# Optimization experiments

Measured on AMD Instinct MI355X. Metric: run time of the kernel, lower is better.

## Reference

```python
import jax, jax.numpy as jnp
import numpy as np

B, S, DIN, DEG = 256, 51, 512, 50
N = B * S           # 13056 nodes
E = N * DEG         # 652800 edges
NEG_SLOPE = 0.01    # torch leaky_relu default
EPS = 1e-12         # torch F.normalize default eps


def setup_inputs() -> dict:
    key = jax.random.key(0)
    ks = iter(jax.random.split(key, 64))

    def p(shape):
        fan_in = shape[0] if len(shape) > 1 else shape[0]
        return jax.random.normal(next(ks), shape, jnp.float32) / np.sqrt(fan_in)

    inp = {
        "x": jax.random.normal(next(ks), (B, S, DIN), jnp.float32),
        "x_pose": jax.random.normal(next(ks), (B, S, 7), jnp.float32),
        # mlp2: in_feats->256->128->64 (ReLU)
        "m2w1": p((DIN, 256)), "m2b1": jnp.zeros((256,), jnp.float32),
        "m2w2": p((256, 128)), "m2b2": jnp.zeros((128,), jnp.float32),
        "m2w3": p((128, 64)),  "m2b3": jnp.zeros((64,), jnp.float32),
        # mlp3: 7->16->32->64 (ReLU)
        "m3w1": p((7, 16)),   "m3b1": jnp.zeros((16,), jnp.float32),
        "m3w2": p((16, 32)),  "m3b2": jnp.zeros((32,), jnp.float32),
        "m3w3": p((32, 64)),  "m3b3": jnp.zeros((64,), jnp.float32),
        # Encoder: 128->256 (ReLU)
        "encw": p((128, 256)), "encb": jnp.zeros((256,), jnp.float32),
        # edge MLP: 256->256->128->64->1 (leaky_relu, sigmoid at end)
        "ew1": p((256, 256)), "eb1": jnp.zeros((256,), jnp.float32),
        "ew2": p((256, 128)), "eb2": jnp.zeros((128,), jnp.float32),
        "ew3": p((128, 64)),  "eb3": jnp.zeros((64,), jnp.float32),
        "ew4": p((64, 1)),    "eb4": jnp.zeros((1,), jnp.float32),
        # SAGEConv(256,128,'mean'): fc_self, fc_neigh, bias
        "wself": p((256, 128)), "wneigh": p((256, 128)),
        "sageb": jnp.zeros((128,), jnp.float32),
        # Decoder: 128->7
        "decw": p((128, 7)), "decb": jnp.zeros((7,), jnp.float32),
        # graph edges (src -> dst)
        "edge_src": jax.random.randint(next(ks), (E,), 0, N, jnp.int32),
        "edge_dst": jax.random.randint(next(ks), (E,), 0, N, jnp.int32),
    }
    return inp


def reference(x, x_pose,
              m2w1, m2b1, m2w2, m2b2, m2w3, m2b3,
              m3w1, m3b1, m3w2, m3b2, m3w3, m3b3,
              encw, encb,
              ew1, eb1, ew2, eb2, ew3, eb3, ew4, eb4,
              wself, wneigh, sageb, decw, decb,
              edge_src, edge_dst):
    relu = jax.nn.relu
    lrelu = lambda h: jax.nn.leaky_relu(h, NEG_SLOPE)

    # node feature encoders
    h = relu(relu(relu(x @ m2w1 + m2b1) @ m2w2 + m2b2) @ m2w3 + m2b3)        # [B,S,64]
    hp = relu(relu(relu(x_pose @ m3w1 + m3b1) @ m3w2 + m3b2) @ m3w3 + m3b3)  # [B,S,64]
    xn = relu(jnp.concatenate([h, hp], axis=2) @ encw + encb)                # [B,S,256]
    xn = xn.reshape(N, 256)                                                  # node feats

    # apply_edges: score = sigmoid(MLP(h_u - h_v))
    d = xn[edge_src] - xn[edge_dst]                                          # [E,256]
    s = lrelu(d @ ew1 + eb1)
    s = lrelu(s @ ew2 + eb2)
    s = lrelu(s @ ew3 + eb3)
    e = jax.nn.sigmoid(s @ ew4 + eb4)                                        # [E,1]

    # SAGEConv mean aggregation with edge weights: mean over in-edges of e*h_u
    msg = e * xn[edge_src]                                                   # [E,256]
    neigh_sum = jax.ops.segment_sum(msg, edge_dst, num_segments=N)           # [N,256]
    deg = jax.ops.segment_sum(jnp.ones((E,), jnp.float32), edge_dst, num_segments=N)
    neigh = neigh_sum / jnp.maximum(deg, 1.0)[:, None]                       # zero-deg -> 0
    A = xn @ wself + neigh @ wneigh + sageb                                  # [N,128]
    A = A.reshape(B, S, 128)

    est_pose = A @ decw + decb                                               # [B,S,7]
    pos_out = est_pose[:, 0, :3]
    ori_out = est_pose[:, 0, 3:]

    A = lrelu(A)
    A = A / jnp.maximum(jnp.linalg.norm(A, axis=1, keepdims=True), EPS)      # F.normalize dim=1
    return (A, e, pos_out, ori_out)
```

## Files before the change

kernel.cpp:

```cpp
#include <hip/hip_runtime.h>
#include <math.h>

#define B_ 256
#define S_ 51
#define NN (B_*S_)
#define DEG_ 50
#define EE (NN*DEG_)
#define NEG_SLOPE 0.01f
#define EPS_ 1e-12f

#define A_SIZE (NN*128)
#define E_OFF  A_SIZE
#define POS_OFF (A_SIZE + EE)
#define ORI_OFF (POS_OFF + B_*3)

typedef __bf16 bf16x8 __attribute__((ext_vector_type(8)));
typedef __bf16 bf16x4 __attribute__((ext_vector_type(4)));
typedef float  f32x4  __attribute__((ext_vector_type(4)));

typedef __attribute__((address_space(1))) const void GVoid;
typedef __attribute__((address_space(3))) void LVoid;

__device__ __forceinline__ float act_apply(float v, int ACT) {
    if (ACT == 1) return fmaxf(v, 0.0f);
    if (ACT == 2) return v > 0.0f ? v : NEG_SLOPE * v;
    return v;
}

template<int ACT, int ACC>
__global__ __launch_bounds__(256) void gemm_kernel(
    const float* __restrict__ A, int lda,
    const float* __restrict__ W, int ldw,
    const float* __restrict__ bias,
    float* __restrict__ C, int ldc,
    int M, int K, int N)
{
    __shared__ float As[32][68];
    __shared__ float Ws[32][68];

    const int tid = threadIdx.x;
    const int tx = tid & 15;
    const int ty = tid >> 4;
    const int m0 = blockIdx.x * 64;
    const int n0 = blockIdx.y * 64;

    float acc[4][4];
#pragma unroll
    for (int i = 0; i < 4; ++i)
#pragma unroll
        for (int j = 0; j < 4; ++j) acc[i][j] = 0.0f;

    const int ktiles = (K + 31) >> 5;
    for (int kt = 0; kt < ktiles; ++kt) {
        const int k0 = kt << 5;
#pragma unroll
        for (int it = 0; it < 8; ++it) {
            int idx = tid + it * 256;
            int kk = idx & 31;
            int r  = idx >> 5;
            float v = 0.0f;
            int gr = m0 + r, gk = k0 + kk;
            if (gr < M && gk < K) v = A[(size_t)gr * lda + gk];
            As[kk][r] = v;
        }
#pragma unroll
        for (int it = 0; it < 8; ++it) {
            int idx = tid + it * 256;
            int c  = idx & 63;
            int kk = idx >> 6;
            float v = 0.0f;
            int gk = k0 + kk, gc = n0 + c;
            if (gk < K && gc < N) v = W[(size_t)gk * ldw + gc];
            Ws[kk][c] = v;
        }
        __syncthreads();
#pragma unroll
        for (int kk = 0; kk < 32; ++kk) {
            float4 av = *(const float4*)&As[kk][ty * 4];
            float4 wv = *(const float4*)&Ws[kk][tx * 4];
            float a[4] = {av.x, av.y, av.z, av.w};
            float w[4] = {wv.x, wv.y, wv.z, wv.w};
#pragma unroll
            for (int i = 0; i < 4; ++i)
#pragma unroll
                for (int j = 0; j < 4; ++j)
                    acc[i][j] = fmaf(a[i], w[j], acc[i][j]);
        }
        __syncthreads();
    }

#pragma unroll
    for (int i = 0; i < 4; ++i) {
        int row = m0 + ty * 4 + i;
        if (row >= M) continue;
#pragma unroll
        for (int j = 0; j < 4; ++j) {
            int col = n0 + tx * 4 + j;
            if (col >= N) continue;
            float v = acc[i][j];
            if (bias) v += bias[col];
            if (ACC) v += C[(size_t)row * ldc + col];
            C[(size_t)row * ldc + col] = act_apply(v, ACT);
        }
    }
}

__global__ __launch_bounds__(256) void pack_w_kernel(
    const float* __restrict__ W, __bf16* __restrict__ Wp, int K, int N)
{
    int t = blockIdx.x * 256 + threadIdx.x;
    if (t >= K * N) return;
    int j    = t & 7;
    int lane = (t >> 3) & 63;
    int rkt  = t >> 9;
    int KT = K >> 5;
    int kt = rkt % KT;
    int cf = rkt / KT;
    int k = kt * 32 + (lane >> 4) * 8 + j;
    int n = cf * 16 + (lane & 15);
    Wp[t] = (__bf16)W[(size_t)k * N + n];
}

__global__ __launch_bounds__(256) void pack_w2_kernel(
    const float* __restrict__ W, __bf16* __restrict__ Wph, __bf16* __restrict__ Wpl,
    int K, int N)
{
    int t = blockIdx.x * 256 + threadIdx.x;
    if (t >= K * N) return;
    int j    = t & 7;
    int lane = (t >> 3) & 63;
    int rkt  = t >> 9;
    int KT = K >> 5;
    int kt = rkt % KT;
    int cf = rkt / KT;
    int k = kt * 32 + (lane >> 4) * 8 + j;
    int n = cf * 16 + (lane & 15);
    float v = W[(size_t)k * N + n];
    __bf16 h = (__bf16)v;
    Wph[t] = h;
    Wpl[t] = (__bf16)(v - (float)h);
}

template<int K, int BN>
__global__ __launch_bounds__(256) void ygemm_kernel(
    const __bf16* __restrict__ A, const __bf16* __restrict__ Wp,
    __bf16* __restrict__ C, int ldc)
{
    constexpr int NCF = BN / 16;
    __shared__ __bf16 As[128 * 32];

    const int tid  = threadIdx.x;
    const int lane = tid & 63;
    const int w    = tid >> 6;
    const int lg   = lane >> 4;
    const int li   = lane & 15;
    const int n_blk = blockIdx.x * BN;
    const int m_blk = blockIdx.y * 128;

    f32x4 acc[2][NCF];
#pragma unroll
    for (int mf = 0; mf < 2; ++mf)
#pragma unroll
        for (int cf = 0; cf < NCF; ++cf)
#pragma unroll
            for (int r = 0; r < 4; ++r) acc[mf][cf][r] = 0.0f;

    const __bf16* WpBase = Wp + ((size_t)(n_blk / 16) * (K / 32)) * 512 + (size_t)lane * 8;

    for (int kt = 0; kt < K / 32; ++kt) {
#pragma unroll
        for (int i = 0; i < 2; ++i) {
            int slot0 = i * 256 + w * 64;
            int s  = slot0 + lane;
            int r  = s >> 2;
            int sl = s & 3;
            int kb = sl ^ ((r >> 1) & 3);
            const __bf16* g = A + (size_t)(m_blk + r) * K + kt * 32 + kb * 8;
            __builtin_amdgcn_global_load_lds((GVoid*)g,
                                             (LVoid*)((char*)As + (size_t)slot0 * 16),
                                             16, 0, 0);
        }
        bf16x8 bf[NCF];
        const __bf16* Wb = WpBase + (size_t)kt * 512;
#pragma unroll
        for (int cf = 0; cf < NCF; ++cf)
            bf[cf] = *(const bf16x8*)(Wb + (size_t)cf * (K / 32) * 512);

        __syncthreads();

        bf16x8 af[2];
#pragma unroll
        for (int mf = 0; mf < 2; ++mf) {
            int row = w * 32 + mf * 16 + li;
            int sl  = lg ^ ((row >> 1) & 3);
            af[mf] = *(const bf16x8*)((const char*)As + (size_t)row * 64 + sl * 16);
        }
#pragma unroll
        for (int mf = 0; mf < 2; ++mf)
#pragma unroll
            for (int cf = 0; cf < NCF; ++cf)
                acc[mf][cf] = __builtin_amdgcn_mfma_f32_16x16x32_bf16(
                    af[mf], bf[cf], acc[mf][cf], 0, 0, 0);
        __syncthreads();
    }

#pragma unroll
    for (int mf = 0; mf < 2; ++mf) {
        int row0 = m_blk + w * 32 + mf * 16 + lg * 4;
#pragma unroll
        for (int cf = 0; cf < NCF; ++cf) {
            int col = n_blk + cf * 16 + li;
#pragma unroll
            for (int r = 0; r < 4; ++r)
                C[(size_t)(row0 + r) * ldc + col] = (__bf16)acc[mf][cf][r];
        }
    }
}

__global__ __launch_bounds__(256) void edge_fused_kernel(
    const __bf16* __restrict__ Yb, const float* __restrict__ eb1,
    const int* __restrict__ src, const int* __restrict__ dst,
    const __bf16* __restrict__ Wp, const float* __restrict__ eb2,
    __bf16* __restrict__ s2, int e0)
{
    constexpr int K = 256, NCF = 8;
    __shared__ __bf16 As[128 * 32];

    const int tid  = threadIdx.x;
    const int lane = tid & 63;
    const int w    = tid >> 6;
    const int lg   = lane >> 4;
    const int li   = lane & 15;
    const int m_blk = blockIdx.x * 128;

    const int sr = tid >> 1;
    const int sh = tid & 1;
    const int e  = e0 + m_blk + sr;
    const __bf16* ys = Yb + (size_t)src[e] * 256;
    const __bf16* yd = Yb + (size_t)dst[e] * 256;
    const int swz = (sr >> 1) & 3;
    char* wp0 = (char*)As + sr * 64 + (((sh * 2)     ^ swz) * 16);
    char* wp1 = (char*)As + sr * 64 + (((sh * 2 + 1) ^ swz) * 16);

    f32x4 acc[2][NCF];
#pragma unroll
    for (int mf = 0; mf < 2; ++mf)
#pragma unroll
        for (int cf = 0; cf < NCF; ++cf)
#pragma unroll
            for (int r = 0; r < 4; ++r) acc[mf][cf][r] = 0.0f;

    const __bf16* WpBase = Wp + (size_t)lane * 8;

    for (int kt = 0; kt < K / 32; ++kt) {
        const int k0 = kt * 32 + sh * 16;
        bf16x8 a0 = *(const bf16x8*)(ys + k0);
        bf16x8 a1 = *(const bf16x8*)(ys + k0 + 8);
        bf16x8 b0 = *(const bf16x8*)(yd + k0);
        bf16x8 b1 = *(const bf16x8*)(yd + k0 + 8);
        bf16x8 o0, o1;
#pragma unroll
        for (int j = 0; j < 8; ++j) {
            float v0 = (float)a0[j] - (float)b0[j] + eb1[k0 + j];
            float v1 = (float)a1[j] - (float)b1[j] + eb1[k0 + 8 + j];
            v0 = v0 > 0.0f ? v0 : NEG_SLOPE * v0;
            v1 = v1 > 0.0f ? v1 : NEG_SLOPE * v1;
            o0[j] = (__bf16)v0;
            o1[j] = (__bf16)v1;
        }
        *(bf16x8*)wp0 = o0;
        *(bf16x8*)wp1 = o1;

        bf16x8 bf[NCF];
        const __bf16* Wb = WpBase + (size_t)kt * 512;
#pragma unroll
        for (int cf = 0; cf < NCF; ++cf)
            bf[cf] = *(const bf16x8*)(Wb + (size_t)cf * (K / 32) * 512);

        __syncthreads();

        bf16x8 af[2];
#pragma unroll
        for (int mf = 0; mf < 2; ++mf) {
            int row = w * 32 + mf * 16 + li;
            int sl  = lg ^ ((row >> 1) & 3);
            af[mf] = *(const bf16x8*)((const char*)As + (size_t)row * 64 + sl * 16);
        }
#pragma unroll
        for (int mf = 0; mf < 2; ++mf)
#pragma unroll
            for (int cf = 0; cf < NCF; ++cf)
                acc[mf][cf] = __builtin_amdgcn_mfma_f32_16x16x32_bf16(
                    af[mf], bf[cf], acc[mf][cf], 0, 0, 0);
        __syncthreads();
    }

    float bv[NCF];
#pragma unroll
    for (int cf = 0; cf < NCF; ++cf) bv[cf] = eb2[cf * 16 + li];
#pragma unroll
    for (int mf = 0; mf < 2; ++mf) {
        int row0 = m_blk + w * 32 + mf * 16 + lg * 4;
#pragma unroll
        for (int cf = 0; cf < NCF; ++cf) {
            int col = cf * 16 + li;
#pragma unroll
            for (int r = 0; r < 4; ++r) {
                float v = acc[mf][cf][r] + bv[cf];
                v = v > 0.0f ? v : NEG_SLOPE * v;
                s2[(size_t)(row0 + r) * 128 + col] = (__bf16)v;
            }
        }
    }
}

__global__ __launch_bounds__(256) void edge_l3e_kernel(
    const __bf16* __restrict__ A, const __bf16* __restrict__ Wp,
    const float* __restrict__ eb3, const float* __restrict__ ew4,
    const float* __restrict__ eb4, float* __restrict__ e_out, int e0)
{
    constexpr int K = 128, NCF = 4;
    __shared__ __bf16 As[128 * 32];

    const int tid  = threadIdx.x;
    const int lane = tid & 63;
    const int w    = tid >> 6;
    const int lg   = lane >> 4;
    const int li   = lane & 15;
    const int m_blk = blockIdx.y * 128;

    f32x4 acc[2][NCF];
#pragma unroll
    for (int mf = 0; mf < 2; ++mf)
#pragma unroll
        for (int cf = 0; cf < NCF; ++cf)
#pragma unroll
            for (int r = 0; r < 4; ++r) acc[mf][cf][r] = 0.0f;

    const __bf16* WpBase = Wp + (size_t)lane * 8;

    for (int kt = 0; kt < K / 32; ++kt) {
#pragma unroll
        for (int i = 0; i < 2; ++i) {
            int slot0 = i * 256 + w * 64;
            int s  = slot0 + lane;
            int r  = s >> 2;
            int sl = s & 3;
            int kb = sl ^ ((r >> 1) & 3);
            const __bf16* g = A + (size_t)(m_blk + r) * K + kt * 32 + kb * 8;
            __builtin_amdgcn_global_load_lds((GVoid*)g,
                                             (LVoid*)((char*)As + (size_t)slot0 * 16),
                                             16, 0, 0);
        }
        bf16x8 bf[NCF];
        const __bf16* Wb = WpBase + (size_t)kt * 512;
#pragma unroll
        for (int cf = 0; cf < NCF; ++cf)
            bf[cf] = *(const bf16x8*)(Wb + (size_t)cf * (K / 32) * 512);

        __syncthreads();

        bf16x8 af[2];
#pragma unroll
        for (int mf = 0; mf < 2; ++mf) {
            int row = w * 32 + mf * 16 + li;
            int sl  = lg ^ ((row >> 1) & 3);
            af[mf] = *(const bf16x8*)((const char*)As + (size_t)row * 64 + sl * 16);
        }
#pragma unroll
        for (int mf = 0; mf < 2; ++mf)
#pragma unroll
            for (int cf = 0; cf < NCF; ++cf)
                acc[mf][cf] = __builtin_amdgcn_mfma_f32_16x16x32_bf16(
                    af[mf], bf[cf], acc[mf][cf], 0, 0, 0);
        __syncthreads();
    }

    float p[2][4];
#pragma unroll
    for (int mf = 0; mf < 2; ++mf)
#pragma unroll
        for (int r = 0; r < 4; ++r) p[mf][r] = 0.0f;
#pragma unroll
    for (int cf = 0; cf < NCF; ++cf) {
        int col = cf * 16 + li;
        float b3 = eb3[col];
        float w4 = ew4[col];
#pragma unroll
        for (int mf = 0; mf < 2; ++mf)
#pragma unroll
            for (int r = 0; r < 4; ++r) {
                float v = acc[mf][cf][r] + b3;
                v = v > 0.0f ? v : NEG_SLOPE * v;
                p[mf][r] = fmaf(v, w4, p[mf][r]);
            }
    }
#pragma unroll
    for (int mf = 0; mf < 2; ++mf)
#pragma unroll
        for (int r = 0; r < 4; ++r) {
#pragma unroll
            for (int m = 1; m < 16; m <<= 1)
                p[mf][r] += __shfl_xor(p[mf][r], m, 16);
        }
    if (li == 0) {
        float b4 = eb4[0];
#pragma unroll
        for (int mf = 0; mf < 2; ++mf)
#pragma unroll
            for (int r = 0; r < 4; ++r) {
                int ei = m_blk + w * 32 + mf * 16 + lg * 4 + r;
                float ev = 1.0f / (1.0f + expf(-(p[mf][r] + b4)));
                e_out[e0 + ei] = ev;
            }
    }
}

template<int K, int BN, int ACT, int OUT, int ACC>
__global__ __launch_bounds__(256) void mmx_kernel(
    const __bf16* __restrict__ Ah, const __bf16* __restrict__ Al,
    const __bf16* __restrict__ Wph, const __bf16* __restrict__ Wpl,
    const float* __restrict__ bias,
    float* __restrict__ Cf, __bf16* __restrict__ Ch, __bf16* __restrict__ Cl, int ldc)
{
    constexpr int NCF = BN / 16;
    __shared__ __bf16 AsH[128 * 32];
    __shared__ __bf16 AsL[128 * 32];

    const int tid  = threadIdx.x;
    const int lane = tid & 63;
    const int w    = tid >> 6;
    const int lg   = lane >> 4;
    const int li   = lane & 15;
    const int n_blk = blockIdx.x * BN;
    const int m_blk = blockIdx.y * 128;

    f32x4 acc[2][NCF];
#pragma unroll
    for (int mf = 0; mf < 2; ++mf)
#pragma unroll
        for (int cf = 0; cf < NCF; ++cf)
#pragma unroll
            for (int r = 0; r < 4; ++r) acc[mf][cf][r] = 0.0f;

    const size_t wbase = ((size_t)(n_blk / 16) * (K / 32)) * 512 + (size_t)lane * 8;

    for (int kt = 0; kt < K / 32; ++kt) {
#pragma unroll
        for (int i = 0; i < 2; ++i) {
            int slot0 = i * 256 + w * 64;
            int s  = slot0 + lane;
            int r  = s >> 2;
            int sl = s & 3;
            int kb = sl ^ ((r >> 1) & 3);
            size_t goff = (size_t)(m_blk + r) * K + kt * 32 + kb * 8;
            __builtin_amdgcn_global_load_lds((GVoid*)(Ah + goff),
                                             (LVoid*)((char*)AsH + (size_t)slot0 * 16),
                                             16, 0, 0);
            __builtin_amdgcn_global_load_lds((GVoid*)(Al + goff),
                                             (LVoid*)((char*)AsL + (size_t)slot0 * 16),
                                             16, 0, 0);
        }
        bf16x8 bfh[NCF], bfl[NCF];
        const size_t wo = wbase + (size_t)kt * 512;
#pragma unroll
        for (int cf = 0; cf < NCF; ++cf) {
            size_t o = wo + (size_t)cf * (K / 32) * 512;
            bfh[cf] = *(const bf16x8*)(Wph + o);
            bfl[cf] = *(const bf16x8*)(Wpl + o);
        }

        __syncthreads();

        bf16x8 afh[2], afl[2];
#pragma unroll
        for (int mf = 0; mf < 2; ++mf) {
            int row = w * 32 + mf * 16 + li;
            int sl  = lg ^ ((row >> 1) & 3);
            afh[mf] = *(const bf16x8*)((const char*)AsH + (size_t)row * 64 + sl * 16);
            afl[mf] = *(const bf16x8*)((const char*)AsL + (size_t)row * 64 + sl * 16);
        }
#pragma unroll
        for (int mf = 0; mf < 2; ++mf)
#pragma unroll
            for (int cf = 0; cf < NCF; ++cf) {
                acc[mf][cf] = __builtin_amdgcn_mfma_f32_16x16x32_bf16(
                    afh[mf], bfh[cf], acc[mf][cf], 0, 0, 0);
                acc[mf][cf] = __builtin_amdgcn_mfma_f32_16x16x32_bf16(
                    afh[mf], bfl[cf], acc[mf][cf], 0, 0, 0);
                acc[mf][cf] = __builtin_amdgcn_mfma_f32_16x16x32_bf16(
                    afl[mf], bfh[cf], acc[mf][cf], 0, 0, 0);
            }
        __syncthreads();
    }

    float bv[NCF];
#pragma unroll
    for (int cf = 0; cf < NCF; ++cf) bv[cf] = bias ? bias[n_blk + cf * 16 + li] : 0.0f;
#pragma unroll
    for (int mf = 0; mf < 2; ++mf) {
        int row0 = m_blk + w * 32 + mf * 16 + lg * 4;
#pragma unroll
        for (int cf = 0; cf < NCF; ++cf) {
            int col = n_blk + cf * 16 + li;
#pragma unroll
            for (int r = 0; r < 4; ++r) {
                float v = acc[mf][cf][r] + bv[cf];
                size_t idx = (size_t)(row0 + r) * ldc + col;
                if (ACC) v += Cf[idx];
                v = act_apply(v, ACT);
                if (OUT & 1) Cf[idx] = v;
                if (OUT & 2) {
                    __bf16 h = (__bf16)v;
                    Ch[idx] = h;
                    Cl[idx] = (__bf16)(v - (float)h);
                }
            }
        }
    }
}

__global__ __launch_bounds__(256) void split_bf16_kernel(
    const float* __restrict__ in, __bf16* __restrict__ hi, __bf16* __restrict__ lo, int n8)
{
    int i = blockIdx.x * 256 + threadIdx.x;
    if (i >= n8) return;
    const float4* p = (const float4*)in + (size_t)i * 2;
    float4 a = p[0], b = p[1];
    float v[8] = {a.x, a.y, a.z, a.w, b.x, b.y, b.z, b.w};
    bf16x8 oh, ol;
#pragma unroll
    for (int j = 0; j < 8; ++j) {
        __bf16 h = (__bf16)v[j];
        oh[j] = h;
        ol[j] = (__bf16)(v[j] - (float)h);
    }
    *(bf16x8*)(hi + (size_t)i * 8) = oh;
    *(bf16x8*)(lo + (size_t)i * 8) = ol;
}

__global__ __launch_bounds__(256) void hist_kernel(
    const int* __restrict__ dst, int* __restrict__ counts)
{
    int e = blockIdx.x * 256 + threadIdx.x;
    if (e < EE) atomicAdd(&counts[dst[e]], 1);
}

__global__ __launch_bounds__(1024) void scan_kernel(
    const int* __restrict__ counts, int* __restrict__ row_start, int* __restrict__ cursor)
{
    __shared__ int buf[1024];
    __shared__ int carry_s;
    int tid = threadIdx.x;
    if (tid == 0) carry_s = 0;
    __syncthreads();
    for (int t0 = 0; t0 < NN; t0 += 1024) {
        int i = t0 + tid;
        int v = (i < NN) ? counts[i] : 0;
        buf[tid] = v;
        __syncthreads();
        int c = carry_s;
        for (int o = 1; o < 1024; o <<= 1) {
            int u = (tid >= o) ? buf[tid - o] : 0;
            __syncthreads();
            buf[tid] += u;
            __syncthreads();
        }
        int excl = buf[tid] - v;
        if (i < NN) { row_start[i] = c + excl; cursor[i] = c + excl; }
        int total = buf[1023];
        __syncthreads();
        if (tid == 0) carry_s = c + total;
        __syncthreads();
    }
}

__global__ __launch_bounds__(256) void scatter_kernel(
    const int* __restrict__ src, const int* __restrict__ dst,
    const float* __restrict__ e_out, int* __restrict__ cursor, int2* __restrict__ bucket)
{
    int e = blockIdx.x * 256 + threadIdx.x;
    if (e >= EE) return;
    int d = dst[e];
    int pos = atomicAdd(&cursor[d], 1);
    bucket[pos] = make_int2(src[e], __float_as_int(e_out[e]));
}

__global__ __launch_bounds__(256) void neigh_gather_kernel(
    const float* __restrict__ xn, const int2* __restrict__ bucket,
    const int* __restrict__ row_start, const int* __restrict__ counts,
    __bf16* __restrict__ nh, __bf16* __restrict__ nl)
{
    __shared__ int2 eb[128];
    int n = blockIdx.x;
    int f = threadIdx.x;
    int s0 = row_start[n];
    int cnt = counts[n];
    float acc = 0.0f;
    for (int t = 0; t < cnt; t += 128) {
        int m = (cnt - t < 128) ? (cnt - t) : 128;
        __syncthreads();
        if (f < m) eb[f] = bucket[s0 + t + f];
        __syncthreads();
        for (int i = 0; i < m; ++i) {
            int2 p = eb[i];
            acc = fmaf(__int_as_float(p.y), xn[(size_t)p.x * 256 + f], acc);
        }
    }
    float dv = (float)(cnt > 0 ? cnt : 1);
    float v = acc / dv;
    __bf16 h = (__bf16)v;
    nh[(size_t)n * 256 + f] = h;
    nl[(size_t)n * 256 + f] = (__bf16)(v - (float)h);
}

__global__ __launch_bounds__(128) void pose_kernel(
    const float* __restrict__ A_pre, const float* __restrict__ decw,
    const float* __restrict__ decb, float* __restrict__ pos, float* __restrict__ ori)
{
    __shared__ float arow[128];
    int b = blockIdx.x;
    arow[threadIdx.x] = A_pre[(size_t)(b * S_) * 128 + threadIdx.x];
    __syncthreads();
    int t = threadIdx.x;
    if (t < 7) {
        float s = decb[t];
        for (int c = 0; c < 128; ++c) s = fmaf(arow[c], decw[c * 7 + t], s);
        if (t < 3) pos[b * 3 + t] = s;
        else       ori[b * 4 + (t - 3)] = s;
    }
}

__global__ __launch_bounds__(128) void norm_kernel(
    const float* __restrict__ A_pre, float* __restrict__ out)
{
    int b = blockIdx.x;
    int c = threadIdx.x;
    size_t base = (size_t)b * S_ * 128 + c;
    float ss = 0.0f;
    for (int s = 0; s < S_; ++s) {
        float v = A_pre[base + (size_t)s * 128];
        v = v > 0.0f ? v : NEG_SLOPE * v;
        ss = fmaf(v, v, ss);
    }
    float nrm = fmaxf(sqrtf(ss), EPS_);
    float inv = 1.0f / nrm;
    for (int s = 0; s < S_; ++s) {
        float v = A_pre[base + (size_t)s * 128];
        v = v > 0.0f ? v : NEG_SLOPE * v;
        out[base + (size_t)s * 128] = v * inv;
    }
}

extern "C" void kernel_launch(void* const* d_in, const int* in_sizes, int n_in,
                              void* d_out, int out_size, void* d_ws, size_t ws_size,
                              hipStream_t stream) {
    const float* x      = (const float*)d_in[0];
    const float* x_pose = (const float*)d_in[1];
    const float* m2w1 = (const float*)d_in[2];
    const float* m2b1 = (const float*)d_in[3];
    const float* m2w2 = (const float*)d_in[4];
    const float* m2b2 = (const float*)d_in[5];
    const float* m2w3 = (const float*)d_in[6];
    const float* m2b3 = (const float*)d_in[7];
    const float* m3w1 = (const float*)d_in[8];
    const float* m3b1 = (const float*)d_in[9];
    const float* m3w2 = (const float*)d_in[10];
    const float* m3b2 = (const float*)d_in[11];
    const float* m3w3 = (const float*)d_in[12];
    const float* m3b3 = (const float*)d_in[13];
    const float* encw = (const float*)d_in[14];
    const float* encb = (const float*)d_in[15];
    const float* ew1  = (const float*)d_in[16];
    const float* eb1  = (const float*)d_in[17];
    const float* ew2  = (const float*)d_in[18];
    const float* eb2  = (const float*)d_in[19];
    const float* ew3  = (const float*)d_in[20];
    const float* eb3  = (const float*)d_in[21];
    const float* ew4  = (const float*)d_in[22];
    const float* eb4  = (const float*)d_in[23];
    const float* wself  = (const float*)d_in[24];
    const float* wneigh = (const float*)d_in[25];
    const float* sageb  = (const float*)d_in[26];
    const float* decw = (const float*)d_in[27];
    const float* decb = (const float*)d_in[28];
    const int* esrc = (const int*)d_in[29];
    const int* edst = (const int*)d_in[30];
    float* out = (float*)d_out;

    char* base = (char*)d_ws;
    size_t off = 0;
    auto alloc = [&](size_t bytes) { char* p = base + off; off += (bytes + 15) & ~15ULL; return p; };
    float* xn        = (float*)alloc((size_t)NN * 256 * 4);
    float* A_pre     = (float*)alloc((size_t)NN * 128 * 4);
    float* p1        = (float*)alloc((size_t)NN * 16 * 4);
    float* p2        = (float*)alloc((size_t)NN * 32 * 4);
    int*  counts    = (int*)alloc((size_t)NN * 4);
    int*  row_start = (int*)alloc((size_t)NN * 4);
    int*  cursor    = (int*)alloc((size_t)NN * 4);
    int2* bucket    = (int2*)alloc((size_t)EE * 8);
    __bf16* Yb   = (__bf16*)alloc((size_t)NN * 256 * 2);
    __bf16* xh   = (__bf16*)alloc((size_t)NN * 512 * 2);
    __bf16* xl   = (__bf16*)alloc((size_t)NN * 512 * 2);
    __bf16* t1h  = (__bf16*)alloc((size_t)NN * 256 * 2);
    __bf16* t1l  = (__bf16*)alloc((size_t)NN * 256 * 2);
    __bf16* t2h  = (__bf16*)alloc((size_t)NN * 128 * 2);
    __bf16* t2l  = (__bf16*)alloc((size_t)NN * 128 * 2);
    __bf16* hch  = (__bf16*)alloc((size_t)NN * 128 * 2);
    __bf16* hcl  = (__bf16*)alloc((size_t)NN * 128 * 2);
    __bf16* p2h  = (__bf16*)alloc((size_t)NN * 32 * 2);
    __bf16* p2l  = (__bf16*)alloc((size_t)NN * 32 * 2);
    __bf16* xnh  = (__bf16*)alloc((size_t)NN * 256 * 2);
    __bf16* xnl  = (__bf16*)alloc((size_t)NN * 256 * 2);
    __bf16* ngh  = (__bf16*)alloc((size_t)NN * 256 * 2);
    __bf16* ngl  = (__bf16*)alloc((size_t)NN * 256 * 2);
    __bf16* wpn1h = (__bf16*)alloc((size_t)512 * 256 * 2);
    __bf16* wpn1l = (__bf16*)alloc((size_t)512 * 256 * 2);
    __bf16* wpn2h = (__bf16*)alloc((size_t)256 * 128 * 2);
    __bf16* wpn2l = (__bf16*)alloc((size_t)256 * 128 * 2);
    __bf16* wpn3h = (__bf16*)alloc((size_t)128 * 64 * 2);
    __bf16* wpn3l = (__bf16*)alloc((size_t)128 * 64 * 2);
    __bf16* wpp3h = (__bf16*)alloc((size_t)32 * 64 * 2);
    __bf16* wpp3l = (__bf16*)alloc((size_t)32 * 64 * 2);
    __bf16* wpenh = (__bf16*)alloc((size_t)128 * 256 * 2);
    __bf16* wpenl = (__bf16*)alloc((size_t)128 * 256 * 2);
    __bf16* wpsfh = (__bf16*)alloc((size_t)256 * 128 * 2);
    __bf16* wpsfl = (__bf16*)alloc((size_t)256 * 128 * 2);
    __bf16* wpngh = (__bf16*)alloc((size_t)256 * 128 * 2);
    __bf16* wpngl = (__bf16*)alloc((size_t)256 * 128 * 2);
    __bf16* wpe1 = (__bf16*)alloc((size_t)256 * 256 * 2);
    __bf16* wpe2 = (__bf16*)alloc((size_t)256 * 128 * 2);
    __bf16* wpe3 = (__bf16*)alloc((size_t)128 * 64 * 2);

    long long avail_bytes = (long long)ws_size - (long long)off;
    const long long PER_EDGE_B = 128 * 2;
    long long ecmax = avail_bytes / PER_EDGE_B;
    ecmax = (ecmax / 128) * 128;
    if (ecmax > EE) ecmax = EE;
    if (ecmax < 128) ecmax = 128;
    int nchunk = (int)((EE + ecmax - 1) / ecmax);
    long long ec = ((EE + nchunk - 1) / nchunk + 127) / 128 * 128;

    __bf16* s2 = (__bf16*)(base + off);

    hipMemsetAsync(counts, 0, (size_t)NN * sizeof(int), stream);

    pack_w2_kernel<<<(512*256+255)/256, 256, 0, stream>>>(m2w1, wpn1h, wpn1l, 512, 256);
    pack_w2_kernel<<<(256*128+255)/256, 256, 0, stream>>>(m2w2, wpn2h, wpn2l, 256, 128);
    pack_w2_kernel<<<(128*64 +255)/256, 256, 0, stream>>>(m2w3, wpn3h, wpn3l, 128, 64);
    pack_w2_kernel<<<(32*64  +255)/256, 256, 0, stream>>>(m3w3, wpp3h, wpp3l, 32, 64);
    pack_w2_kernel<<<(128*256+255)/256, 256, 0, stream>>>(encw, wpenh, wpenl, 128, 256);
    pack_w2_kernel<<<(256*128+255)/256, 256, 0, stream>>>(wself, wpsfh, wpsfl, 256, 128);
    pack_w2_kernel<<<(256*128+255)/256, 256, 0, stream>>>(wneigh, wpngh, wpngl, 256, 128);
    pack_w_kernel<<<(256*256+255)/256, 256, 0, stream>>>(ew1, wpe1, 256, 256);
    pack_w_kernel<<<(256*128+255)/256, 256, 0, stream>>>(ew2, wpe2, 256, 128);
    pack_w_kernel<<<(128*64 +255)/256, 256, 0, stream>>>(ew3, wpe3, 128, 64);

    split_bf16_kernel<<<(NN*512/8 + 255)/256, 256, 0, stream>>>(x, xh, xl, NN*512/8);

    const dim3 blk(256, 1, 1);
    const int MB = NN / 128;

    mmx_kernel<512,64,1,2,0><<<dim3(4, MB), blk, 0, stream>>>(xh, xl, wpn1h, wpn1l, m2b1, nullptr, t1h, t1l, 256);
    mmx_kernel<256,64,1,2,0><<<dim3(2, MB), blk, 0, stream>>>(t1h, t1l, wpn2h, wpn2l, m2b2, nullptr, t2h, t2l, 128);
    mmx_kernel<128,64,1,2,0><<<dim3(1, MB), blk, 0, stream>>>(t2h, t2l, wpn3h, wpn3l, m2b3, nullptr, hch, hcl, 128);

    gemm_kernel<1,0><<<dim3((NN+63)/64, 1), blk, 0, stream>>>(x_pose, 7,  m3w1, 16, m3b1, p1, 16, NN, 7, 16);
    gemm_kernel<1,0><<<dim3((NN+63)/64, 1), blk, 0, stream>>>(p1,    16,  m3w2, 32, m3b2, p2, 32, NN, 16, 32);
    split_bf16_kernel<<<(NN*32/8 + 255)/256, 256, 0, stream>>>(p2, p2h, p2l, NN*32/8);
    mmx_kernel< 32,64,1,2,0><<<dim3(1, MB), blk, 0, stream>>>(p2h, p2l, wpp3h, wpp3l, m3b3, nullptr, hch + 64, hcl + 64, 128);

    mmx_kernel<128,64,1,3,0><<<dim3(4, MB), blk, 0, stream>>>(hch, hcl, wpenh, wpenl, encb, xn, xnh, xnl, 256);

    ygemm_kernel<256,128><<<dim3(2, MB), blk, 0, stream>>>(xnh, wpe1, Yb, 256);

    for (int c = 0; c < nchunk; ++c) {
        long long e0 = (long long)c * ec;
        int ecc = (int)((e0 + ec <= EE) ? ec : (EE - e0));
        edge_fused_kernel<<<dim3(ecc / 128), blk, 0, stream>>>(
            Yb, eb1, esrc, edst, wpe2, eb2, s2, (int)e0);
        edge_l3e_kernel<<<dim3(1, ecc / 128), blk, 0, stream>>>(
            s2, wpe3, eb3, ew4, eb4, out + E_OFF, (int)e0);
    }

    hist_kernel<<<(EE + 255) / 256, 256, 0, stream>>>(edst, counts);
    scan_kernel<<<1, 1024, 0, stream>>>(counts, row_start, cursor);
    scatter_kernel<<<(EE + 255) / 256, 256, 0, stream>>>(esrc, edst, out + E_OFF, cursor, bucket);
    neigh_gather_kernel<<<NN, 256, 0, stream>>>(xn, bucket, row_start, counts, ngh, ngl);

    mmx_kernel<256,64,0,1,0><<<dim3(2, MB), blk, 0, stream>>>(xnh, xnl, wpsfh, wpsfl, sageb,  A_pre, nullptr, nullptr, 128);
    mmx_kernel<256,64,0,1,1><<<dim3(2, MB), blk, 0, stream>>>(ngh, ngl, wpngh, wpngl, nullptr, A_pre, nullptr, nullptr, 128);

    pose_kernel<<<B_, 128, 0, stream>>>(A_pre, decw, decb, out + POS_OFF, out + ORI_OFF);
    norm_kernel<<<B_, 128, 0, stream>>>(A_pre, out);
}
```

Before: 632.7 us.

## Fuse edge MLP layers 2-4 into one kernel keeping layer-2 output in LDS

Merges the layer-2 edge kernel and the layer-3/4 sigmoid kernel into a single kernel that writes the 128x128 bf16 intermediate into a swizzled shared-memory tile instead of global memory. This removes the global write and re-read of the [E,128] intermediate, along with the chunking logic and the extra launches. The cost is 32KB of extra LDS per block, which may lower occupancy, plus a longer kernel with an extra barrier.

```diff
diff --git a/kernel.cpp b/kernel.cpp
--- a/kernel.cpp
+++ b/kernel.cpp
@@ -217,14 +217,17 @@
     }
 }
 
-__global__ __launch_bounds__(256) void edge_fused_kernel(
+__global__ __launch_bounds__(256) void edge_full_kernel(
     const __bf16* __restrict__ Yb, const float* __restrict__ eb1,
     const int* __restrict__ src, const int* __restrict__ dst,
-    const __bf16* __restrict__ Wp, const float* __restrict__ eb2,
-    __bf16* __restrict__ s2, int e0)
+    const __bf16* __restrict__ Wp2, const float* __restrict__ eb2,
+    const __bf16* __restrict__ Wp3, const float* __restrict__ eb3,
+    const float* __restrict__ ew4, const float* __restrict__ eb4,
+    float* __restrict__ e_out)
 {
     constexpr int K = 256, NCF = 8;
     __shared__ __bf16 As[128 * 32];
+    __shared__ __bf16 S2[128 * 128];
 
     const int tid  = threadIdx.x;
     const int lane = tid & 63;
@@ -235,7 +238,7 @@
 
     const int sr = tid >> 1;
     const int sh = tid & 1;
-    const int e  = e0 + m_blk + sr;
+    const int e  = m_blk + sr;
     const __bf16* ys = Yb + (size_t)src[e] * 256;
     const __bf16* yd = Yb + (size_t)dst[e] * 256;
     const int swz = (sr >> 1) & 3;
@@ -250,7 +253,7 @@
 #pragma unroll
             for (int r = 0; r < 4; ++r) acc[mf][cf][r] = 0.0f;
 
-    const __bf16* WpBase = Wp + (size_t)lane * 8;
+    const __bf16* WpBase2 = Wp2 + (size_t)lane * 8;
 
     for (int kt = 0; kt < K / 32; ++kt) {
         const int k0 = kt * 32 + sh * 16;
@@ -272,7 +275,7 @@
         *(bf16x8*)wp1 = o1;
 
         bf16x8 bf[NCF];
-        const __bf16* Wb = WpBase + (size_t)kt * 512;
+        const __bf16* Wb = WpBase2 + (size_t)kt * 512;
 #pragma unroll
         for (int cf = 0; cf < NCF; ++cf)
             bf[cf] = *(const bf16x8*)(Wb + (size_t)cf * (K / 32) * 512);
@@ -295,85 +298,56 @@
         __syncthreads();
     }
 
-    float bv[NCF];
-#pragma unroll
-    for (int cf = 0; cf < NCF; ++cf) bv[cf] = eb2[cf * 16 + li];
 #pragma unroll
     for (int mf = 0; mf < 2; ++mf) {
-        int row0 = m_blk + w * 32 + mf * 16 + lg * 4;
+        int row0 = w * 32 + mf * 16 + lg * 4;
 #pragma unroll
         for (int cf = 0; cf < NCF; ++cf) {
             int col = cf * 16 + li;
+            float bv = eb2[col];
+            int sl = col >> 3;
+            int sb = col & 7;
 #pragma unroll
             for (int r = 0; r < 4; ++r) {
-                float v = acc[mf][cf][r] + bv[cf];
+                int row = row0 + r;
+                float v = acc[mf][cf][r] + bv;
                 v = v > 0.0f ? v : NEG_SLOPE * v;
-                s2[(size_t)(row0 + r) * 128 + col] = (__bf16)v;
+                S2[row * 128 + ((sl ^ (row & 7)) << 3) + sb] = (__bf16)v;
             }
         }
     }
-}
-
-__global__ __launch_bounds__(256) void edge_l3e_kernel(
-    const __bf16* __restrict__ A, const __bf16* __restrict__ Wp,
-    const float* __restrict__ eb3, const float* __restrict__ ew4,
-    const float* __restrict__ eb4, float* __restrict__ e_out, int e0)
-{
-    constexpr int K = 128, NCF = 4;
-    __shared__ __bf16 As[128 * 32];
-
-    const int tid  = threadIdx.x;
-    const int lane = tid & 63;
-    const int w    = tid >> 6;
-    const int lg   = lane >> 4;
-    const int li   = lane & 15;
-    const int m_blk = blockIdx.y * 128;
-
-    f32x4 acc[2][NCF];
+    __syncthreads();
+
+    constexpr int NCF3 = 4;
+    f32x4 acc3[2][NCF3];
 #pragma unroll
     for (int mf = 0; mf < 2; ++mf)
 #pragma unroll
-        for (int cf = 0; cf < NCF; ++cf)
-#pragma unroll
-            for (int r = 0; r < 4; ++r) acc[mf][cf][r] = 0.0f;
-
-    const __bf16* WpBase = Wp + (size_t)lane * 8;
-
-    for (int kt = 0; kt < K / 32; ++kt) {
-#pragma unroll
-        for (int i = 0; i < 2; ++i) {
-            int slot0 = i * 256 + w * 64;
-            int s  = slot0 + lane;
-            int r  = s >> 2;
-            int sl = s & 3;
-            int kb = sl ^ ((r >> 1) & 3);
-            const __bf16* g = A + (size_t)(m_blk + r) * K + kt * 32 + kb * 8;
-            __builtin_amdgcn_global_load_lds((GVoid*)g,
-                                             (LVoid*)((char*)As + (size_t)slot0 * 16),
-                                             16, 0, 0);
-        }
-        bf16x8 bf[NCF];
-        const __bf16* Wb = WpBase + (size_t)kt * 512;
-#pragma unroll
-        for (int cf = 0; cf < NCF; ++cf)
-            bf[cf] = *(const bf16x8*)(Wb + (size_t)cf * (K / 32) * 512);
-
-        __syncthreads();
-
+        for (int cf = 0; cf < NCF3; ++cf)
+#pragma unroll
+            for (int r = 0; r < 4; ++r) acc3[mf][cf][r] = 0.0f;
+
+    const __bf16* WpBase3 = Wp3 + (size_t)lane * 8;
+#pragma unroll
+    for (int kt = 0; kt < 4; ++kt) {
         bf16x8 af[2];
 #pragma unroll
         for (int mf = 0; mf < 2; ++mf) {
             int row = w * 32 + mf * 16 + li;
-            int sl  = lg ^ ((row >> 1) & 3);
-            af[mf] = *(const bf16x8*)((const char*)As + (size_t)row * 64 + sl * 16);
-        }
+            int sl  = (kt * 4 + lg) ^ (row & 7);
+            af[mf] = *(const bf16x8*)&S2[row * 128 + (sl << 3)];
+        }
+        bf16x8 bf[NCF3];
+        const __bf16* Wb = WpBase3 + (size_t)kt * 512;
+#pragma unroll
+        for (int cf = 0; cf < NCF3; ++cf)
+            bf[cf] = *(const bf16x8*)(Wb + (size_t)cf * 4 * 512);
 #pragma unroll
         for (int mf = 0; mf < 2; ++mf)
 #pragma unroll
-            for (int cf = 0; cf < NCF; ++cf)
-                acc[mf][cf] = __builtin_amdgcn_mfma_f32_16x16x32_bf16(
-                    af[mf], bf[cf], acc[mf][cf], 0, 0, 0);
-        __syncthreads();
+            for (int cf = 0; cf < NCF3; ++cf)
+                acc3[mf][cf] = __builtin_amdgcn_mfma_f32_16x16x32_bf16(
+                    af[mf], bf[cf], acc3[mf][cf], 0, 0, 0);
     }
 
     float p[2][4];
@@ -382,7 +356,7 @@
 #pragma unroll
         for (int r = 0; r < 4; ++r) p[mf][r] = 0.0f;
 #pragma unroll
-    for (int cf = 0; cf < NCF; ++cf) {
+    for (int cf = 0; cf < NCF3; ++cf) {
         int col = cf * 16 + li;
         float b3 = eb3[col];
         float w4 = ew4[col];
@@ -390,7 +364,7 @@
         for (int mf = 0; mf < 2; ++mf)
 #pragma unroll
             for (int r = 0; r < 4; ++r) {
-                float v = acc[mf][cf][r] + b3;
+                float v = acc3[mf][cf][r] + b3;
                 v = v > 0.0f ? v : NEG_SLOPE * v;
                 p[mf][r] = fmaf(v, w4, p[mf][r]);
             }
@@ -411,7 +385,7 @@
             for (int r = 0; r < 4; ++r) {
                 int ei = m_blk + w * 32 + mf * 16 + lg * 4 + r;
                 float ev = 1.0f / (1.0f + expf(-(p[mf][r] + b4)));
-                e_out[e0 + ei] = ev;
+                e_out[ei] = ev;
             }
     }
 }
@@ -732,17 +706,6 @@
     __bf16* wpe2 = (__bf16*)alloc((size_t)256 * 128 * 2);
     __bf16* wpe3 = (__bf16*)alloc((size_t)128 * 64 * 2);
 
-    long long avail_bytes = (long long)ws_size - (long long)off;
-    const long long PER_EDGE_B = 128 * 2;
-    long long ecmax = avail_bytes / PER_EDGE_B;
-    ecmax = (ecmax / 128) * 128;
-    if (ecmax > EE) ecmax = EE;
-    if (ecmax < 128) ecmax = 128;
-    int nchunk = (int)((EE + ecmax - 1) / ecmax);
-    long long ec = ((EE + nchunk - 1) / nchunk + 127) / 128 * 128;
-
-    __bf16* s2 = (__bf16*)(base + off);
-
     hipMemsetAsync(counts, 0, (size_t)NN * sizeof(int), stream);
 
     pack_w2_kernel<<<(512*256+255)/256, 256, 0, stream>>>(m2w1, wpn1h, wpn1l, 512, 256);
@@ -774,14 +737,8 @@
 
     ygemm_kernel<256,128><<<dim3(2, MB), blk, 0, stream>>>(xnh, wpe1, Yb, 256);
 
-    for (int c = 0; c < nchunk; ++c) {
-        long long e0 = (long long)c * ec;
-        int ecc = (int)((e0 + ec <= EE) ? ec : (EE - e0));
-        edge_fused_kernel<<<dim3(ecc / 128), blk, 0, stream>>>(
-            Yb, eb1, esrc, edst, wpe2, eb2, s2, (int)e0);
-        edge_l3e_kernel<<<dim3(1, ecc / 128), blk, 0, stream>>>(
-            s2, wpe3, eb3, ew4, eb4, out + E_OFF, (int)e0);
-    }
+    edge_full_kernel<<<dim3(EE / 128), blk, 0, stream>>>(
+        Yb, eb1, esrc, edst, wpe2, eb2, wpe3, eb3, ew4, eb4, out + E_OFF);
 
     hist_kernel<<<(EE + 255) / 256, 256, 0, stream>>>(edst, counts);
     scan_kernel<<<1, 1024, 0, stream>>>(counts, row_start, cursor);
```

New measurement: 632.0 us. Within noise of the previous version (-0.1%).
